# Optimization experiments

Measured on AMD Instinct MI355X. Metric: run time of the kernel, lower is better.

Reference implementation:

```python
import jax, jax.numpy as jnp
import numpy as np

NUM_HEADS = 16
HEAD_DIM = 64  # hidden_size 1024 / 16 heads


def setup_inputs() -> dict:
    key = jax.random.key(0)
    k1, k2, k3, k4 = jax.random.split(key, 4)
    B, S, H = 2, 2048, 1024
    qkv = jax.random.normal(k1, (B, S, H), dtype=jnp.float32)
    # True = masked position (tf.where(mask, -inf, scores))
    mask = jax.random.bernoulli(k2, 0.5, (B, S))
    Wqkv = jax.random.normal(k3, (H, 3 * H), dtype=jnp.float32) * (H ** -0.5)
    bqkv = jnp.zeros((3 * H,), dtype=jnp.float32)
    Wo = jax.random.normal(k4, (H, H), dtype=jnp.float32) * (H ** -0.5)
    bo = jnp.zeros((H,), dtype=jnp.float32)
    return {"qkv": qkv, "mask": mask, "Wqkv": Wqkv, "bqkv": bqkv, "Wo": Wo, "bo": bo}


def reference(qkv, mask, Wqkv, bqkv, Wo, bo):
    B, S, H = qkv.shape
    nh, hd = NUM_HEADS, HEAD_DIM
    proj = qkv @ Wqkv + bqkv                       # (B,S,3H)
    q, k, v = jnp.split(proj, 3, axis=-1)
    # NOTE: original MULTIPLIES query by sqrt(head_dim) (faithful to source)
    q = q * (hd ** 0.5)
    q = q.reshape(B, S, nh, hd).transpose(0, 2, 1, 3)   # (B,h,S,d)
    k = k.reshape(B, S, nh, hd).transpose(0, 2, 1, 3)
    v = v.reshape(B, S, nh, hd).transpose(0, 2, 1, 3)
    scores = jnp.einsum("bhqd,bhkd->bhqk", q, k)        # (B,h,S,S)
    scores = jnp.where(mask[:, None, None, :], -jnp.inf, scores)
    attn = jax.nn.softmax(scores, axis=-1)              # dropout identity at inference
    out = jnp.einsum("bhqk,bhkd->bhqd", attn, v)        # (B,h,S,d)
    out = out.transpose(0, 2, 1, 3).reshape(B, S, H)
    return out @ Wo + bo
```

## Files before the change

kernel.cpp:

```cpp
#include <hip/hip_runtime.h>

#define DEV __device__ __forceinline__

typedef unsigned short u16;
typedef unsigned int u32;
typedef __attribute__((ext_vector_type(4))) float f32x4;
typedef __attribute__((ext_vector_type(8))) short s16x8;
typedef __attribute__((ext_vector_type(8))) _Float16 f16x8;
typedef __attribute__((ext_vector_type(4))) unsigned short u16x4;
typedef __attribute__((ext_vector_type(4))) unsigned int u32x4;

#define BATCH 2
#define SEQ 2048
#define HID 1024
#define NH 16
#define HD 64

#define SCALE_XW 64.0f
#define INV_PROJ (1.0f / 4096.0f)
#define SCALE_Q 11.541560327111707f
#define SCALE_K 1.0f
#define DEFER_THR 10.0f

DEV f32x4 mfmah(s16x8 a, s16x8 b, f32x4 c) {
    return __builtin_amdgcn_mfma_f32_16x16x32_f16(
        __builtin_bit_cast(f16x8, a), __builtin_bit_cast(f16x8, b), c, 0, 0, 0);
}

DEV u16 f2h(float x) { return __builtin_bit_cast(u16, (_Float16)x); }
DEV float h2f(u16 h) { return (float)__builtin_bit_cast(_Float16, h); }

DEV u32 pkh(float a, float b) {
#if __has_builtin(__builtin_amdgcn_cvt_pkrtz)
    auto r = __builtin_amdgcn_cvt_pkrtz(a, b);
    return __builtin_bit_cast(u32, r);
#else
    return (u32)f2h(a) | ((u32)f2h(b) << 16);
#endif
}

DEV float fexp2(float x) {
#if __has_builtin(__builtin_amdgcn_exp2f)
    return __builtin_amdgcn_exp2f(x);
#else
    return exp2f(x);
#endif
}

DEV void swap32(int lane, u32 a, u32 b, u32& o0, u32& o1) {
#if __has_builtin(__builtin_amdgcn_permlane32_swap)
    auto r = __builtin_amdgcn_permlane32_swap((int)a, (int)b, false, false);
    o0 = (u32)r[0]; o1 = (u32)r[1];
#else
    u32 ax = (u32)__shfl_xor((int)a, 32);
    u32 bx = (u32)__shfl_xor((int)b, 32);
    bool hi = (lane & 32) != 0;
    o0 = hi ? bx : a;
    o1 = hi ? b : ax;
#endif
}
DEV void swap16(int lane, u32 a, u32 b, u32& o0, u32& o1) {
#if __has_builtin(__builtin_amdgcn_permlane16_swap)
    auto r = __builtin_amdgcn_permlane16_swap((int)a, (int)b, false, false);
    o0 = (u32)r[0]; o1 = (u32)r[1];
#else
    u32 ax = (u32)__shfl_xor((int)a, 16);
    u32 bx = (u32)__shfl_xor((int)b, 16);
    bool hi = (lane & 16) != 0;
    o0 = hi ? bx : a;
    o1 = hi ? b : ax;
#endif
}

DEV void gl_lds16(const void* g, void* l) {
    __builtin_amdgcn_global_load_lds(
        (__attribute__((address_space(1))) void*)(void*)g,
        (__attribute__((address_space(3))) void*)l, 16, 0, 0);
}

DEV void vm0_bar() {
    __builtin_amdgcn_sched_barrier(0);
    asm volatile("s_waitcnt vmcnt(0)" ::: "memory");
    __builtin_amdgcn_s_barrier();
    __builtin_amdgcn_sched_barrier(0);
}

DEV s16x8 lds_ld16(const u16* base, int row, int kbyte) {
    return *(const s16x8*)((const char*)base + row * 128 + (kbyte ^ ((row & 7) << 4)));
}
DEV s16x8 lds_ld32r(const u16* base, int row, int g) {
    return *(const s16x8*)((const char*)base + row * 64 + ((g * 16) ^ ((row & 3) << 4)));
}

__global__ __launch_bounds__(256) void prep_all(
    const float* __restrict__ qkv, const unsigned char* __restrict__ m,
    const float* __restrict__ Wqkv, const float* __restrict__ Wo,
    u16* __restrict__ Xh, u16* __restrict__ Wth, u16* __restrict__ Woth,
    float* __restrict__ pbias, int* __restrict__ pack_idx, int* __restrict__ cnt) {
    int bid = blockIdx.x;
    int tid = threadIdx.x;
    if (bid == 0) {
        __shared__ int sb, sf;
        __shared__ int scan[256];
        if (tid == 0) { sb = 0; sf = 0; }
        __syncthreads();
        int lb = 0, lf = 0;
        for (int i = tid * 16; i < tid * 16 + 16; i++) {
            unsigned char v = m[i];
            int pos = i & 3;
            if (pos == 3 && v == 0x3f) lf = 1;
            if (pos != 0 && v != 0) lb = 1;
        }
        if (lb) atomicOr(&sb, 1);
        if (lf) atomicOr(&sf, 1);
        __syncthreads();
        int f = sf ? 2 : (sb ? 1 : 0);
#pragma unroll
        for (int b = 0; b < BATCH; b++) {
            int base = b * SEQ;
            int keep[8], lc = 0;
#pragma unroll
            for (int e = 0; e < 8; e++) {
                int i = base + tid * 8 + e;
                int mv;
                if (f == 0) mv = ((const int*)m)[i] != 0;
                else if (f == 1) mv = m[i] != 0;
                else mv = ((const float*)m)[i] != 0.0f;
                keep[e] = !mv;
                lc += keep[e];
            }
            scan[tid] = lc;
            __syncthreads();
            for (int s = 1; s < 256; s <<= 1) {
                int v = (tid >= s) ? scan[tid - s] : 0;
                __syncthreads();
                scan[tid] += v;
                __syncthreads();
            }
            int off = scan[tid] - lc;
            int total = scan[255];
            __syncthreads();
#pragma unroll
            for (int e = 0; e < 8; e++)
                if (keep[e]) pack_idx[base + off++] = base + tid * 8 + e;
            if (tid == 0) cnt[b] = total;
            for (int j = tid; j < SEQ; j += 256)
                pbias[base + j] = (j < total) ? 0.0f : -1e30f;
        }
    } else if (bid <= 3072 + 1024) {
        const float* in;
        u16* oh;
        int N, t;
        float scale;
        if (bid <= 3072) { in = Wqkv; oh = Wth; N = 3072; t = bid - 1; scale = SCALE_XW; }
        else { in = Wo; oh = Woth; N = 1024; t = bid - 3073; scale = 1.0f; }
        const int K = 1024;
        int ntiles = N >> 5;
        int n0 = (t % ntiles) * 32, k0 = (t / ntiles) * 32;
        __shared__ float tt[32][33];
        int tx = tid & 31, ty = tid >> 5;
#pragma unroll
        for (int i = 0; i < 4; i++)
            tt[ty + 8 * i][tx] = in[(size_t)(k0 + ty + 8 * i) * N + n0 + tx];
        __syncthreads();
#pragma unroll
        for (int i = 0; i < 4; i++) {
            float v = tt[tx][ty + 8 * i] * scale;
            size_t o = (size_t)(n0 + ty + 8 * i) * K + k0 + tx;
            oh[o] = f2h(v);
        }
    } else {
        int cb = bid - 3073 - 1024;
#pragma unroll
        for (int it = 0; it < 4; it++) {
            int i = ((cb + it * 1024) * 256 + tid) * 4;
            f32x4 v = *(const f32x4*)&qkv[i];
            u16x4 h;
#pragma unroll
            for (int e = 0; e < 4; e++) h[e] = f2h(v[e] * SCALE_XW);
            *(u16x4*)&Xh[i] = h;
        }
    }
}

__global__ __launch_bounds__(256, 3) void gemm_qkv(
    const u16* __restrict__ Xh,
    const u16* __restrict__ Wth,
    const float* __restrict__ bqkv,
    const int* __restrict__ pack_idx, const int* __restrict__ cnt,
    u16* __restrict__ qh,
    u16* __restrict__ kh,
    u16* __restrict__ vt) {
    __shared__ __align__(16) u16 SM[2][128 * 32];
    __shared__ __align__(16) u16 T[64 * 140];
    int tid = threadIdx.x, lane = tid & 63, w = tid >> 6;
    int g = lane >> 4, q15 = lane & 15;
    int wm = w >> 1, wn = w & 1;
    int m0 = blockIdx.y * 128, n0 = blockIdx.x * 128;
    int part = n0 >> 10;
    int bb = m0 >> 11;
    int cb = cnt[bb];
    if (part != 0 && (m0 & 2047) >= cb) return;

    int srcrow[2];
#pragma unroll
    for (int i = 0; i < 2; i++) {
        int r = m0 + ((i * 256 + tid) >> 2);
        srcrow[i] = (part == 0) ? r : (((r & 2047) < cb) ? pack_idx[r] : (bb << 11));
    }

    f32x4 acc[4][4];
#pragma unroll
    for (int i = 0; i < 4; i++)
#pragma unroll
        for (int j = 0; j < 4; j++) acc[i][j] = (f32x4){0.f, 0.f, 0.f, 0.f};

    auto STAGE = [&](int kt) {
        int k0 = kt * 32;
#pragma unroll
        for (int i = 0; i < 2; i++) {
            int c = i * 256 + tid;
            int row = c >> 2, slot = c & 3;
            int sg = slot ^ (row & 3);
            int dst = (c & ~63) * 8;
            size_t ga = (size_t)srcrow[i] * 1024 + k0 + sg * 8;
            size_t gb = (size_t)(n0 + row) * 1024 + k0 + sg * 8;
            gl_lds16(&Xh[ga], &SM[0][dst]);
            gl_lds16(&Wth[gb], &SM[1][dst]);
        }
    };

    STAGE(0);
    for (int kt = 0; kt < 32; kt++) {
        vm0_bar();
        s16x8 a_h[4], b_h[4];
#pragma unroll
        for (int i = 0; i < 4; i++) {
            a_h[i] = lds_ld32r(SM[0], wm * 64 + i * 16 + q15, g);
            b_h[i] = lds_ld32r(SM[1], wn * 64 + i * 16 + q15, g);
        }
        __syncthreads();
        if (kt < 31) STAGE(kt + 1);
#pragma unroll
        for (int mi = 0; mi < 4; mi++)
#pragma unroll
            for (int ni = 0; ni < 4; ni++)
                acc[mi][ni] = mfmah(a_h[mi], b_h[ni], acc[mi][ni]);
    }

    if (part == 2) {
        const int TP = 140;
#pragma unroll
        for (int h2 = 0; h2 < 2; h2++) {
            __syncthreads();
            if (wn == h2) {
#pragma unroll
                for (int mi = 0; mi < 4; mi++)
#pragma unroll
                    for (int ni = 0; ni < 4; ni++) {
                        int lcol = ni * 16 + q15;
#pragma unroll
                        for (int j = 0; j < 4; j++) {
                            int lrow = wm * 64 + mi * 16 + g * 4 + j;
                            T[lcol * TP + lrow] =
                                f2h(acc[mi][ni][j] * INV_PROJ + bqkv[n0 + h2 * 64 + lcol]);
                        }
                    }
            }
            __syncthreads();
            int lcol = tid >> 2;
            int seg = tid & 3;
            int c = n0 - 2048 + h2 * 64 + lcol;
            int h = c >> 6, d = c & 63;
            int b = m0 >> 11, sbase = m0 & 2047;
            size_t rowbase = ((size_t)(b * NH + h) * HD + d) * SEQ + sbase;
#pragma unroll
            for (int k = 0; k < 2; k++) {
                int slot = seg * 2 + k;
                *(s16x8*)&vt[rowbase + slot * 16 + 0] = *(const s16x8*)&T[lcol * TP + slot * 16 + 0];
                *(s16x8*)&vt[rowbase + slot * 16 + 8] = *(const s16x8*)&T[lcol * TP + slot * 16 + 8];
            }
        }
    } else {
#pragma unroll
        for (int mi = 0; mi < 4; mi++)
#pragma unroll
            for (int ni = 0; ni < 4; ni++) {
                int col = n0 + wn * 64 + ni * 16 + q15;
                float bias = bqkv[col];
                int cc = col & 1023, h = cc >> 6, d = cc & 63;
#pragma unroll
                for (int j = 0; j < 4; j++) {
                    int row = m0 + wm * 64 + mi * 16 + g * 4 + j;
                    int b = row >> 11, s = row & 2047;
                    float v = acc[mi][ni][j] * INV_PROJ + bias;
                    v *= (part == 0) ? SCALE_Q : SCALE_K;
                    size_t o = (size_t)(b * NH + h) * SEQ * HD + (size_t)s * HD + d;
                    if (part == 0) qh[o] = f2h(v);
                    else kh[o] = f2h(v);
                }
            }
    }
}

__global__ __launch_bounds__(256, 2) void attn_kernel(
    const u16* __restrict__ qh,
    const u16* __restrict__ kh,
    const u16* __restrict__ vt, const float* __restrict__ pbias,
    const int* __restrict__ cnt,
    u16* __restrict__ att) {
    __shared__ __align__(16) u16 Kh[2][4096], Vt[2][4096];
    __shared__ __align__(16) float MskB[2][64];
    int tid = threadIdx.x, lane = tid & 63, w = tid >> 6;
    int g = lane >> 4, q15 = lane & 15;
    int bid = blockIdx.y * 16 + blockIdx.x;
    int swz = (bid & 7) * 64 + (bid >> 3);
    int qt = swz & 15, bh = swz >> 4;
    int b = bh >> 4, h = bh & 15;
    int q0 = qt * 128;
    int NT = (cnt[b] + 63) >> 6;
    size_t base = (size_t)bh * SEQ * HD;
    const u16* vbase = vt + (size_t)bh * HD * SEQ;
    const float* mrow = pbias + b * SEQ;

    s16x8 aq[2][2];
#pragma unroll
    for (int grp = 0; grp < 2; grp++)
#pragma unroll
        for (int k2 = 0; k2 < 2; k2++) {
            size_t o = base + (size_t)(q0 + w * 32 + grp * 16 + q15) * HD + k2 * 32 + g * 8;
            aq[grp][k2] = *(const s16x8*)&qh[o];
        }

    float m_[2] = {-1e30f, -1e30f}, l_[2] = {0.f, 0.f};
    f32x4 o_[2][4];
#pragma unroll
    for (int grp = 0; grp < 2; grp++)
#pragma unroll
        for (int df = 0; df < 4; df++) o_[grp][df] = (f32x4){0.f, 0.f, 0.f, 0.f};

    auto STAGE = [&](int buf, int k0) {
#pragma unroll
        for (int i = 0; i < 2; i++) {
            int c = i * 256 + tid;
            int row = c >> 3, slot = c & 7;
            int sg = slot ^ (row & 7);
            int dst = (c & ~63) * 8;
            size_t gK = base + (size_t)(k0 + row) * HD + sg * 8;
            gl_lds16(&kh[gK], &Kh[buf][dst]);
            size_t gV = (size_t)row * SEQ + k0 + sg * 8;
            gl_lds16(&vbase[gV], &Vt[buf][dst]);
        }
        if (tid < 16) gl_lds16(&mrow[k0 + tid * 4], &MskB[buf][0]);
    };

    STAGE(0, 0);
    __syncthreads();

    for (int kt = 0; kt < NT; kt++) {
        int cur = kt & 1;
        if (kt < NT - 1) STAGE(cur ^ 1, (kt + 1) * 64);

        f32x4 sc0[4], sc1[4];
#pragma unroll
        for (int nf = 0; nf < 4; nf++) {
            f32x4 mb = *(const f32x4*)&MskB[cur][nf * 16 + g * 4];
            sc0[nf] = mb;
            sc1[nf] = mb;
        }
#pragma unroll
        for (int nf = 0; nf < 4; nf++) {
#pragma unroll
            for (int k2 = 0; k2 < 2; k2++) {
                int kb = k2 * 64 + g * 16;
                s16x8 kbh = lds_ld16(Kh[cur], nf * 16 + q15, kb);
                sc0[nf] = mfmah(kbh, aq[0][k2], sc0[nf]);
                sc1[nf] = mfmah(kbh, aq[1][k2], sc1[nf]);
            }
        }

        s16x8 pa[2][2];
#pragma unroll
        for (int grp = 0; grp < 2; grp++) {
            f32x4* sc = grp ? sc1 : sc0;
            float pml = -1e30f;
#pragma unroll
            for (int nf = 0; nf < 4; nf++) {
                float a = fmaxf(sc[nf][0], sc[nf][1]);
                float bmx = fmaxf(sc[nf][2], sc[nf][3]);
                pml = fmaxf(pml, fmaxf(a, bmx));
            }
            if (!__all(pml - m_[grp] <= DEFER_THR)) {
                float pm = fmaxf(pml, __shfl_xor(pml, 16));
                pm = fmaxf(pm, __shfl_xor(pm, 32));
                float mn = fmaxf(m_[grp], pm);
                float scl = fexp2(m_[grp] - mn);
                m_[grp] = mn;
                l_[grp] *= scl;
#pragma unroll
                for (int j = 0; j < 4; j++) {
                    float sb = __shfl(scl, g * 4 + j);
#pragma unroll
                    for (int df = 0; df < 4; df++) o_[grp][df][j] *= sb;
                }
            }
            float p[4][4];
            float rs = 0.f;
#pragma unroll
            for (int nf = 0; nf < 4; nf++)
#pragma unroll
                for (int j = 0; j < 4; j++) {
                    float pv = fexp2(sc[nf][j] - m_[grp]);
                    p[nf][j] = pv;
                    rs += pv;
                }
            l_[grp] += rs;
#pragma unroll
            for (int k2 = 0; k2 < 2; k2++) {
                u32 A0 = pkh(p[2 * k2][0], p[2 * k2][1]);
                u32 A1 = pkh(p[2 * k2][2], p[2 * k2][3]);
                u32 B0 = pkh(p[2 * k2 + 1][0], p[2 * k2 + 1][1]);
                u32 B1 = pkh(p[2 * k2 + 1][2], p[2 * k2 + 1][3]);
                u32 s0, s1, t0, t1, w0, w1, w2, w3;
                swap32(lane, A0, B0, s0, s1);
                swap16(lane, s0, s1, w0, w2);
                swap32(lane, A1, B1, t0, t1);
                swap16(lane, t0, t1, w1, w3);
                u32x4 words = {w0, w1, w2, w3};
                pa[grp][k2] = __builtin_bit_cast(s16x8, words);
            }
        }

#pragma unroll
        for (int k2 = 0; k2 < 2; k2++) {
            int kb = k2 * 64 + g * 16;
#pragma unroll
            for (int df = 0; df < 4; df++) {
                s16x8 vb = lds_ld16(Vt[cur], df * 16 + q15, kb);
                o_[0][df] = mfmah(pa[0][k2], vb, o_[0][df]);
                o_[1][df] = mfmah(pa[1][k2], vb, o_[1][df]);
            }
        }
        __syncthreads();
    }

#pragma unroll
    for (int grp = 0; grp < 2; grp++) {
        float lt = l_[grp];
        lt += __shfl_xor(lt, 16);
        lt += __shfl_xor(lt, 32);
#pragma unroll
        for (int j = 0; j < 4; j++) {
            float lb = __shfl(lt, g * 4 + j);
            float linv = __builtin_amdgcn_rcpf(lb);
            int qrow = q0 + w * 32 + grp * 16 + g * 4 + j;
            size_t srow = (size_t)(b * SEQ + qrow);
#pragma unroll
            for (int df = 0; df < 4; df++) {
                int col = h * HD + df * 16 + q15;
                att[srow * HID + col] = f2h(o_[grp][df][j] * linv);
            }
        }
    }
}

__global__ __launch_bounds__(256, 4) void gemm_out(
    const u16* __restrict__ A, const u16* __restrict__ Bh0,
    const float* __restrict__ bo, float* __restrict__ out) {
    __shared__ __align__(16) u16 SMa[2][64 * 32], SMb[2][128 * 32];
    int tid = threadIdx.x, lane = tid & 63, w = tid >> 6;
    int g = lane >> 4, q15 = lane & 15;
    int wm = w >> 1, wn = w & 1;
    int m0 = blockIdx.y * 64, n0 = blockIdx.x * 128;
    f32x4 acc[2][4];
#pragma unroll
    for (int i = 0; i < 2; i++)
#pragma unroll
        for (int j = 0; j < 4; j++) acc[i][j] = (f32x4){0.f, 0.f, 0.f, 0.f};

    auto STAGE = [&](int db, int kt) {
        int k0 = kt * 32;
        {
            int c = tid;
            int row = c >> 2, slot = c & 3;
            int sg = slot ^ (row & 3);
            int dst = (c & ~63) * 8;
            gl_lds16(&A[(size_t)(m0 + row) * 1024 + k0 + sg * 8], &SMa[db][dst]);
        }
#pragma unroll
        for (int i = 0; i < 2; i++) {
            int c = i * 256 + tid;
            int row = c >> 2, slot = c & 3;
            int sg = slot ^ (row & 3);
            int dst = (c & ~63) * 8;
            gl_lds16(&Bh0[(size_t)(n0 + row) * 1024 + k0 + sg * 8], &SMb[db][dst]);
        }
    };

    STAGE(0, 0);
    for (int kt = 0; kt < 32; kt++) {
        int cur = kt & 1;
        __syncthreads();
        if (kt < 31) STAGE(cur ^ 1, kt + 1);
        s16x8 a_[2], b_[4];
#pragma unroll
        for (int i = 0; i < 2; i++)
            a_[i] = lds_ld32r(SMa[cur], wm * 32 + i * 16 + q15, g);
#pragma unroll
        for (int i = 0; i < 4; i++)
            b_[i] = lds_ld32r(SMb[cur], wn * 64 + i * 16 + q15, g);
#pragma unroll
        for (int mi = 0; mi < 2; mi++)
#pragma unroll
            for (int ni = 0; ni < 4; ni++)
                acc[mi][ni] = mfmah(a_[mi], b_[ni], acc[mi][ni]);
    }
#pragma unroll
    for (int mi = 0; mi < 2; mi++)
#pragma unroll
        for (int ni = 0; ni < 4; ni++) {
            int col = n0 + wn * 64 + ni * 16 + q15;
            float bias = bo[col];
#pragma unroll
            for (int j = 0; j < 4; j++) {
                int row = m0 + wm * 32 + mi * 16 + g * 4 + j;
                out[(size_t)row * 1024 + col] = acc[mi][ni][j] + bias;
            }
        }
}

extern "C" void kernel_launch(void* const* d_in, const int* in_sizes, int n_in,
                              void* d_out, int out_size, void* d_ws, size_t ws_size,
                              hipStream_t stream) {
    const float* qkv = (const float*)d_in[0];
    const void* mask = d_in[1];
    const float* Wqkv = (const float*)d_in[2];
    const float* bqkv = (const float*)d_in[3];
    const float* Wo = (const float*)d_in[4];
    const float* bo = (const float*)d_in[5];
    float* out = (float*)d_out;

    const size_t SZ_X = (size_t)4096 * 1024 * 2;
    const size_t SZ_W = (size_t)3072 * 1024 * 2;
    const size_t SZ_WO = (size_t)1024 * 1024 * 2;
    const size_t SZ_QKV = (size_t)32 * 2048 * 64 * 2;
    const size_t SZ_ATT = (size_t)4096 * 1024 * 2;

    char* p = (char*)d_ws;
    u16* Xh = (u16*)p; p += SZ_X;
    u16* Wth = (u16*)p; p += SZ_W;
    u16* Woth = (u16*)p; p += SZ_WO;
    u16* qh = (u16*)p; p += SZ_QKV;
    u16* kh = (u16*)p; p += SZ_QKV;
    u16* vt = (u16*)p; p += SZ_QKV;
    u16* att = (u16*)p; p += SZ_ATT;
    float* pbias = (float*)p; p += BATCH * SEQ * 4;
    int* pack_idx = (int*)p; p += BATCH * SEQ * 4;
    int* cnt = (int*)p; p += 256;

    prep_all<<<1 + 3072 + 1024 + 1024, 256, 0, stream>>>(
        qkv, (const unsigned char*)mask, Wqkv, Wo, Xh, Wth, Woth, pbias, pack_idx, cnt);
    gemm_qkv<<<dim3(24, 32), 256, 0, stream>>>(Xh, Wth, bqkv, pack_idx, cnt, qh, kh, vt);
    attn_kernel<<<dim3(16, 32), 256, 0, stream>>>(qh, kh, vt, pbias, cnt, att);
    gemm_out<<<dim3(8, 64), 256, 0, stream>>>(att, Woth, bo, out);
}
```

Measured before the change: 103.1 us.

## Split attention block into 8 waves of 16 query rows each

The attention kernel now launches 512 threads per block instead of 256. Each of the 8 waves handles one 16-row query group instead of two, so per-wave registers (accumulators, scores, P fragments) are halved. K/V staging is spread over twice as many threads, with one load per thread. This aims to raise wave-level parallelism and latency hiding. In exchange, each wave gets less reuse of every K/V fragment read from LDS, and LDS read traffic per block doubles.

After: 99.66 us. 1.03x faster.

```diff
diff --git a/kernel.cpp b/kernel.cpp
--- a/kernel.cpp
+++ b/kernel.cpp
@@ -303,7 +303,7 @@
     }
 }
 
-__global__ __launch_bounds__(256, 2) void attn_kernel(
+__global__ __launch_bounds__(512, 4) void attn_kernel(
     const u16* __restrict__ qh,
     const u16* __restrict__ kh,
     const u16* __restrict__ vt, const float* __restrict__ pbias,
@@ -323,34 +323,26 @@
     const u16* vbase = vt + (size_t)bh * HD * SEQ;
     const float* mrow = pbias + b * SEQ;
 
-    s16x8 aq[2][2];
-#pragma unroll
-    for (int grp = 0; grp < 2; grp++)
-#pragma unroll
-        for (int k2 = 0; k2 < 2; k2++) {
-            size_t o = base + (size_t)(q0 + w * 32 + grp * 16 + q15) * HD + k2 * 32 + g * 8;
-            aq[grp][k2] = *(const s16x8*)&qh[o];
-        }
-
-    float m_[2] = {-1e30f, -1e30f}, l_[2] = {0.f, 0.f};
-    f32x4 o_[2][4];
-#pragma unroll
-    for (int grp = 0; grp < 2; grp++)
-#pragma unroll
-        for (int df = 0; df < 4; df++) o_[grp][df] = (f32x4){0.f, 0.f, 0.f, 0.f};
+    s16x8 aq[2];
+#pragma unroll
+    for (int k2 = 0; k2 < 2; k2++) {
+        size_t o = base + (size_t)(q0 + w * 16 + q15) * HD + k2 * 32 + g * 8;
+        aq[k2] = *(const s16x8*)&qh[o];
+    }
+
+    float m_ = -1e30f, l_ = 0.f;
+    f32x4 o_[4];
+#pragma unroll
+    for (int df = 0; df < 4; df++) o_[df] = (f32x4){0.f, 0.f, 0.f, 0.f};
 
     auto STAGE = [&](int buf, int k0) {
-#pragma unroll
-        for (int i = 0; i < 2; i++) {
-            int c = i * 256 + tid;
-            int row = c >> 3, slot = c & 7;
-            int sg = slot ^ (row & 7);
-            int dst = (c & ~63) * 8;
-            size_t gK = base + (size_t)(k0 + row) * HD + sg * 8;
-            gl_lds16(&kh[gK], &Kh[buf][dst]);
-            size_t gV = (size_t)row * SEQ + k0 + sg * 8;
-            gl_lds16(&vbase[gV], &Vt[buf][dst]);
-        }
+        int row = tid >> 3, slot = tid & 7;
+        int sg = slot ^ (row & 7);
+        int dst = (tid & ~63) * 8;
+        size_t gK = base + (size_t)(k0 + row) * HD + sg * 8;
+        gl_lds16(&kh[gK], &Kh[buf][dst]);
+        size_t gV = (size_t)row * SEQ + k0 + sg * 8;
+        gl_lds16(&vbase[gV], &Vt[buf][dst]);
         if (tid < 16) gl_lds16(&mrow[k0 + tid * 4], &MskB[buf][0]);
     };
 
@@ -361,74 +353,65 @@
         int cur = kt & 1;
         if (kt < NT - 1) STAGE(cur ^ 1, (kt + 1) * 64);
 
-        f32x4 sc0[4], sc1[4];
-#pragma unroll
-        for (int nf = 0; nf < 4; nf++) {
-            f32x4 mb = *(const f32x4*)&MskB[cur][nf * 16 + g * 4];
-            sc0[nf] = mb;
-            sc1[nf] = mb;
-        }
-#pragma unroll
-        for (int nf = 0; nf < 4; nf++) {
+        f32x4 sc[4];
+#pragma unroll
+        for (int nf = 0; nf < 4; nf++)
+            sc[nf] = *(const f32x4*)&MskB[cur][nf * 16 + g * 4];
+#pragma unroll
+        for (int nf = 0; nf < 4; nf++)
 #pragma unroll
             for (int k2 = 0; k2 < 2; k2++) {
                 int kb = k2 * 64 + g * 16;
                 s16x8 kbh = lds_ld16(Kh[cur], nf * 16 + q15, kb);
-                sc0[nf] = mfmah(kbh, aq[0][k2], sc0[nf]);
-                sc1[nf] = mfmah(kbh, aq[1][k2], sc1[nf]);
-            }
-        }
-
-        s16x8 pa[2][2];
-#pragma unroll
-        for (int grp = 0; grp < 2; grp++) {
-            f32x4* sc = grp ? sc1 : sc0;
-            float pml = -1e30f;
-#pragma unroll
-            for (int nf = 0; nf < 4; nf++) {
-                float a = fmaxf(sc[nf][0], sc[nf][1]);
-                float bmx = fmaxf(sc[nf][2], sc[nf][3]);
-                pml = fmaxf(pml, fmaxf(a, bmx));
-            }
-            if (!__all(pml - m_[grp] <= DEFER_THR)) {
-                float pm = fmaxf(pml, __shfl_xor(pml, 16));
-                pm = fmaxf(pm, __shfl_xor(pm, 32));
-                float mn = fmaxf(m_[grp], pm);
-                float scl = fexp2(m_[grp] - mn);
-                m_[grp] = mn;
-                l_[grp] *= scl;
-#pragma unroll
-                for (int j = 0; j < 4; j++) {
-                    float sb = __shfl(scl, g * 4 + j);
-#pragma unroll
-                    for (int df = 0; df < 4; df++) o_[grp][df][j] *= sb;
-                }
-            }
-            float p[4][4];
-            float rs = 0.f;
-#pragma unroll
-            for (int nf = 0; nf < 4; nf++)
-#pragma unroll
-                for (int j = 0; j < 4; j++) {
-                    float pv = fexp2(sc[nf][j] - m_[grp]);
-                    p[nf][j] = pv;
-                    rs += pv;
-                }
-            l_[grp] += rs;
-#pragma unroll
-            for (int k2 = 0; k2 < 2; k2++) {
-                u32 A0 = pkh(p[2 * k2][0], p[2 * k2][1]);
-                u32 A1 = pkh(p[2 * k2][2], p[2 * k2][3]);
-                u32 B0 = pkh(p[2 * k2 + 1][0], p[2 * k2 + 1][1]);
-                u32 B1 = pkh(p[2 * k2 + 1][2], p[2 * k2 + 1][3]);
-                u32 s0, s1, t0, t1, w0, w1, w2, w3;
-                swap32(lane, A0, B0, s0, s1);
-                swap16(lane, s0, s1, w0, w2);
-                swap32(lane, A1, B1, t0, t1);
-                swap16(lane, t0, t1, w1, w3);
-                u32x4 words = {w0, w1, w2, w3};
-                pa[grp][k2] = __builtin_bit_cast(s16x8, words);
-            }
+                sc[nf] = mfmah(kbh, aq[k2], sc[nf]);
+            }
+
+        float pml = -1e30f;
+#pragma unroll
+        for (int nf = 0; nf < 4; nf++) {
+            float a = fmaxf(sc[nf][0], sc[nf][1]);
+            float bmx = fmaxf(sc[nf][2], sc[nf][3]);
+            pml = fmaxf(pml, fmaxf(a, bmx));
+        }
+        if (!__all(pml - m_ <= DEFER_THR)) {
+            float pm = fmaxf(pml, __shfl_xor(pml, 16));
+            pm = fmaxf(pm, __shfl_xor(pm, 32));
+            float mn = fmaxf(m_, pm);
+            float scl = fexp2(m_ - mn);
+            m_ = mn;
+            l_ *= scl;
+#pragma unroll
+            for (int j = 0; j < 4; j++) {
+                float sb = __shfl(scl, g * 4 + j);
+#pragma unroll
+                for (int df = 0; df < 4; df++) o_[df][j] *= sb;
+            }
+        }
+        float p[4][4];
+        float rs = 0.f;
+#pragma unroll
+        for (int nf = 0; nf < 4; nf++)
+#pragma unroll
+            for (int j = 0; j < 4; j++) {
+                float pv = fexp2(sc[nf][j] - m_);
+                p[nf][j] = pv;
+                rs += pv;
+            }
+        l_ += rs;
+        s16x8 pa[2];
+#pragma unroll
+        for (int k2 = 0; k2 < 2; k2++) {
+            u32 A0 = pkh(p[2 * k2][0], p[2 * k2][1]);
+            u32 A1 = pkh(p[2 * k2][2], p[2 * k2][3]);
+            u32 B0 = pkh(p[2 * k2 + 1][0], p[2 * k2 + 1][1]);
+            u32 B1 = pkh(p[2 * k2 + 1][2], p[2 * k2 + 1][3]);
+            u32 s0, s1, t0, t1, w0, w1, w2, w3;
+            swap32(lane, A0, B0, s0, s1);
+            swap16(lane, s0, s1, w0, w2);
+            swap32(lane, A1, B1, t0, t1);
+            swap16(lane, t0, t1, w1, w3);
+            u32x4 words = {w0, w1, w2, w3};
+            pa[k2] = __builtin_bit_cast(s16x8, words);
         }
 
 #pragma unroll
@@ -437,29 +420,25 @@
 #pragma unroll
             for (int df = 0; df < 4; df++) {
                 s16x8 vb = lds_ld16(Vt[cur], df * 16 + q15, kb);
-                o_[0][df] = mfmah(pa[0][k2], vb, o_[0][df]);
-                o_[1][df] = mfmah(pa[1][k2], vb, o_[1][df]);
+                o_[df] = mfmah(pa[k2], vb, o_[df]);
             }
         }
         __syncthreads();
     }
 
-#pragma unroll
-    for (int grp = 0; grp < 2; grp++) {
-        float lt = l_[grp];
-        lt += __shfl_xor(lt, 16);
-        lt += __shfl_xor(lt, 32);
-#pragma unroll
-        for (int j = 0; j < 4; j++) {
-            float lb = __shfl(lt, g * 4 + j);
-            float linv = __builtin_amdgcn_rcpf(lb);
-            int qrow = q0 + w * 32 + grp * 16 + g * 4 + j;
-            size_t srow = (size_t)(b * SEQ + qrow);
-#pragma unroll
-            for (int df = 0; df < 4; df++) {
-                int col = h * HD + df * 16 + q15;
-                att[srow * HID + col] = f2h(o_[grp][df][j] * linv);
-            }
+    float lt = l_;
+    lt += __shfl_xor(lt, 16);
+    lt += __shfl_xor(lt, 32);
+#pragma unroll
+    for (int j = 0; j < 4; j++) {
+        float lb = __shfl(lt, g * 4 + j);
+        float linv = __builtin_amdgcn_rcpf(lb);
+        int qrow = q0 + w * 16 + g * 4 + j;
+        size_t srow = (size_t)(b * SEQ + qrow);
+#pragma unroll
+        for (int df = 0; df < 4; df++) {
+            int col = h * HD + df * 16 + q15;
+            att[srow * HID + col] = f2h(o_[df][j] * linv);
         }
     }
 }
@@ -561,6 +540,6 @@
     prep_all<<<1 + 3072 + 1024 + 1024, 256, 0, stream>>>(
         qkv, (const unsigned char*)mask, Wqkv, Wo, Xh, Wth, Woth, pbias, pack_idx, cnt);
     gemm_qkv<<<dim3(24, 32), 256, 0, stream>>>(Xh, Wth, bqkv, pack_idx, cnt, qh, kh, vt);
-    attn_kernel<<<dim3(16, 32), 256, 0, stream>>>(qh, kh, vt, pbias, cnt, att);
+    attn_kernel<<<dim3(16, 32), 512, 0, stream>>>(qh, kh, vt, pbias, cnt, att);
     gemm_out<<<dim3(8, 64), 256, 0, stream>>>(att, Woth, bo, out);
 }
```
